# Optimization experiments

Measured on AMD Instinct MI355X. Metric: run time of the kernel, lower is better.

Reference implementation:

```python
import jax, jax.numpy as jnp
import numpy as np

THETA = 10000.0
NUM_HEADS = 16


def _rope(x, pos, theta):
    # x: [..., T, d_k], pos: [T]
    d_k = x.shape[-1]
    inv_freq = 1.0 / theta ** (jnp.arange(0, d_k, 2, dtype=jnp.float32) / d_k)
    ang = pos.astype(jnp.float32)[:, None] * inv_freq  # [T, d_k/2]
    cos, sin = jnp.cos(ang), jnp.sin(ang)
    x1, x2 = x[..., ::2], x[..., 1::2]
    even = x1 * cos - x2 * sin
    odd = x1 * sin + x2 * cos
    return jnp.stack([even, odd], axis=-1).reshape(x.shape)


def setup_inputs() -> dict:
    key = jax.random.key(0)
    ks = jax.random.split(key, 5)
    B, T, D = 4, 2048, 1024
    return {
        "in_features": jax.random.normal(ks[0], (B, T, D), dtype=jnp.float32),
        "token_positions": jnp.arange(T, dtype=jnp.int64 if jax.config.jax_enable_x64 else jnp.int32),
        "Wq": jax.random.normal(ks[1], (D, D), dtype=jnp.float32) * 0.02,
        "Wk": jax.random.normal(ks[2], (D, D), dtype=jnp.float32) * 0.02,
        "Wv": jax.random.normal(ks[3], (D, D), dtype=jnp.float32) * 0.02,
        "Wo": jax.random.normal(ks[4], (D, D), dtype=jnp.float32) * 0.02,
    }


def reference(in_features, token_positions, Wq, Wk, Wv, Wo):
    B, T, D = in_features.shape
    h = NUM_HEADS
    d_k = D // h
    # projections (weight stored [out, in], torch applies x @ W.T)
    Q = in_features @ Wq.T
    K = in_features @ Wk.T
    V = in_features @ Wv.T
    # [B, T, h*d_k] -> [B, h, T, d_k]
    Q = Q.reshape(B, T, h, d_k).transpose(0, 2, 1, 3)
    K = K.reshape(B, T, h, d_k).transpose(0, 2, 1, 3)
    V = V.reshape(B, T, h, d_k).transpose(0, 2, 1, 3)
    Q = _rope(Q, token_positions, THETA)
    K = _rope(K, token_positions, THETA)
    scores = jnp.einsum("bhqd,bhkd->bhqk", Q, K) / jnp.sqrt(jnp.float32(d_k))
    causal = jnp.tril(jnp.ones((T, T), dtype=bool))
    scores = jnp.where(causal, scores, -jnp.inf)
    attn = jax.nn.softmax(scores, axis=-1)
    heads = jnp.einsum("bhqk,bhkd->bhqd", attn, V)
    out = heads.transpose(0, 2, 1, 3).reshape(B, T, D)
    return out @ Wo.T
```

## Files before the change

kernel.cpp:

```cpp
#include <hip/hip_runtime.h>


typedef unsigned short u16;
typedef short short8 __attribute__((ext_vector_type(8)));
typedef float f32x4 __attribute__((ext_vector_type(4)));

#if defined(__has_builtin)
#if __has_builtin(__builtin_amdgcn_exp2f)
#define EXP2(x) __builtin_amdgcn_exp2f(x)
#else
#define EXP2(x) exp2f(x)
#endif
#else
#define EXP2(x) exp2f(x)
#endif

#define QSCALE 0.18033688011112042f
#define NEG_L2T_32 -0.4152410118609203f

__device__ __forceinline__ float bf2f(u16 u) {
  return __uint_as_float(((unsigned int)u) << 16);
}
__device__ __forceinline__ u16 f2bf(float f) {
  unsigned int x = __float_as_uint(f);
  x += 0x7fff + ((x >> 16) & 1);
  return (u16)(x >> 16);
}

__device__ __forceinline__ void glds16(const u16* g, u16* l) {
  __builtin_amdgcn_global_load_lds(
      (const __attribute__((address_space(1))) unsigned int*)g,
      (__attribute__((address_space(3))) unsigned int*)l, 16, 0, 0);
}

__global__ __launch_bounds__(256) void cvt_all(
    const float* __restrict__ X, const float* __restrict__ Wq,
    const float* __restrict__ Wk, const float* __restrict__ Wv,
    const float* __restrict__ Wo, u16* __restrict__ Xb,
    u16* __restrict__ Wqkvb, u16* __restrict__ Wob) {
  const int gid = blockIdx.x * 256 + threadIdx.x;
  const int i = gid * 8;
  const int M1 = 1 << 20;
  const float* src;
  u16* dst;
  int off;
  if (i < 8 * M1)        { src = X;  dst = Xb;            off = 0; }
  else if (i < 9 * M1)   { src = Wq; dst = Wqkvb;         off = 8 * M1; }
  else if (i < 10 * M1)  { src = Wk; dst = Wqkvb + M1;    off = 9 * M1; }
  else if (i < 11 * M1)  { src = Wv; dst = Wqkvb + 2*M1;  off = 10 * M1; }
  else                   { src = Wo; dst = Wob;           off = 11 * M1; }
  const int j = i - off;
  const float4 a = *(const float4*)(src + j);
  const float4 b = *(const float4*)(src + j + 4);
  short8 o;
  o[0] = (short)f2bf(a.x); o[1] = (short)f2bf(a.y);
  o[2] = (short)f2bf(a.z); o[3] = (short)f2bf(a.w);
  o[4] = (short)f2bf(b.x); o[5] = (short)f2bf(b.y);
  o[6] = (short)f2bf(b.z); o[7] = (short)f2bf(b.w);
  *(short8*)(dst + j) = o;
}

__global__ __launch_bounds__(256) void gemm_qkv(const u16* __restrict__ A,
                                                const u16* __restrict__ W,
                                                const int* __restrict__ pos,
                                                u16* __restrict__ Qr,
                                                u16* __restrict__ Kr,
                                                u16* __restrict__ Vd) {
  const int K = 1024;
  __shared__ __align__(16) u16 As[128 * 64];
  __shared__ __align__(16) u16 Bs[128 * 64];
  const int tid = threadIdx.x;
  const int m0 = blockIdx.y << 7;
  const int n0 = blockIdx.x << 7;
  const int w = tid >> 6, L = tid & 63;
  const int wm = (w >> 1) << 6, wn = (w & 1) << 6;
  const int lane15 = L & 15, quad = L >> 4;

  f32x4 acc[4][4] = {};

  const u16* Ap[4]; const u16* Bp[4];
  u16* Al[4]; u16* Bl[4];
#pragma unroll
  for (int i = 0; i < 4; ++i) {
    const int s = tid + (i << 8);
    const int row = s >> 3;
    const int c = ((s & 7) ^ (row & 7)) << 3;
    Ap[i] = A + (size_t)(m0 + row) * K + c;
    Bp[i] = W + (size_t)(n0 + row) * K + c;
    Al[i] = &As[s * 8];
    Bl[i] = &Bs[s * 8];
  }

  int offA[4][2], offB[4][2];
#pragma unroll
  for (int mt = 0; mt < 4; ++mt) {
    const int ra = wm + mt * 16 + lane15;
    const int rb = wn + mt * 16 + lane15;
    offA[mt][0] = ra * 64 + ((quad ^ (ra & 7)) << 3);
    offA[mt][1] = ra * 64 + (((quad + 4) ^ (ra & 7)) << 3);
    offB[mt][0] = rb * 64 + ((quad ^ (rb & 7)) << 3);
    offB[mt][1] = rb * 64 + (((quad + 4) ^ (rb & 7)) << 3);
  }

  for (int k0 = 0; k0 < K; k0 += 64) {
    __syncthreads();
#pragma unroll
    for (int i = 0; i < 4; ++i) glds16(Ap[i] + k0, Al[i]);
#pragma unroll
    for (int i = 0; i < 4; ++i) glds16(Bp[i] + k0, Bl[i]);
    __syncthreads();
#pragma unroll
    for (int ks = 0; ks < 2; ++ks) {
      short8 a[4], b[4];
#pragma unroll
      for (int mt = 0; mt < 4; ++mt) a[mt] = *(const short8*)&As[offA[mt][ks]];
#pragma unroll
      for (int nt = 0; nt < 4; ++nt) b[nt] = *(const short8*)&Bs[offB[nt][ks]];
#pragma unroll
      for (int mt = 0; mt < 4; ++mt)
#pragma unroll
        for (int nt = 0; nt < 4; ++nt)
          acc[mt][nt] =
              __builtin_amdgcn_mfma_f32_16x16x32_bf16(a[mt], b[nt], acc[mt][nt], 0, 0, 0);
    }
  }

  const int sel = n0 >> 10;
  const int ncol0 = (n0 & 1023) + wn;
  if (sel == 2) {
#pragma unroll
    for (int mt = 0; mt < 4; ++mt) {
      const int rbase = m0 + wm + mt * 16 + (quad << 2);
#pragma unroll
      for (int nt = 0; nt < 4; ++nt) {
        const int col = ncol0 + nt * 16 + lane15;
#pragma unroll
        for (int r = 0; r < 4; ++r)
          Vd[(size_t)(rbase + r) * 1024 + col] = f2bf(acc[mt][nt][r]);
      }
    }
  } else {
    u16* dst = sel ? Kr : Qr;
    const float sc = sel ? 1.0f : QSCALE;
    float invf[4];
#pragma unroll
    for (int nt = 0; nt < 4; ++nt) {
      const int d2 = ((ncol0 + nt * 16 + lane15) & 63) >> 1;
      invf[nt] = EXP2((float)d2 * NEG_L2T_32);
    }
#pragma unroll
    for (int mt = 0; mt < 4; ++mt) {
      const int rbase = m0 + wm + mt * 16 + (quad << 2);
#pragma unroll
      for (int r = 0; r < 4; ++r) {
        const int m = rbase + r;
        const int bb = m >> 11, tt = m & 2047;
        const float posf = (float)pos[tt];
#pragma unroll
        for (int nt = 0; nt < 4; ++nt) {
          const int col = ncol0 + nt * 16 + lane15;
          const int h = col >> 6, dcol = col & 63;
          float sn, cn;
          __sincosf(posf * invf[nt], &sn, &cn);
          const float self = acc[mt][nt][r];
          const float part = __shfl_xor(self, 1, 64);
          const float res = (dcol & 1) ? (part * sn + self * cn)
                                       : (self * cn - part * sn);
          dst[(((size_t)((bb * 16 + h) * 2048 + tt)) << 6) + dcol] = f2bf(res * sc);
        }
      }
    }
  }
}

__global__ __launch_bounds__(256) void gemm_bt(const u16* __restrict__ A,
                                               const u16* __restrict__ B,
                                               float* __restrict__ C,
                                               int M, int N, int K) {
  __shared__ __align__(16) u16 As[64 * 32];
  __shared__ __align__(16) u16 Bs[128 * 32];
  const int tid = threadIdx.x;
  const int m0 = blockIdx.y << 6;
  const int n0 = blockIdx.x << 7;
  const int w = tid >> 6, L = tid & 63;
  const int wm = (w >> 1) << 5, wn = (w & 1) << 6;
  const int lane15 = L & 15, quad = L >> 4;
  const int koff = quad << 3;

  f32x4 acc[2][4] = {};

  const int s0 = tid, s1 = tid + 256;
  const u16* A0 = A + (size_t)(m0 + (s0 >> 2)) * K + ((s0 & 3) << 3);
  const u16* B0 = B + (size_t)(n0 + (s0 >> 2)) * K + ((s0 & 3) << 3);
  const u16* B1 = B + (size_t)(n0 + (s1 >> 2)) * K + ((s1 & 3) << 3);
  u16* asd0 = &As[s0 * 8];
  u16* bsd0 = &Bs[s0 * 8]; u16* bsd1 = &Bs[s1 * 8];

  for (int k0 = 0; k0 < K; k0 += 32) {
    __syncthreads();
    glds16(A0 + k0, asd0);
    glds16(B0 + k0, bsd0);
    glds16(B1 + k0, bsd1);
    __syncthreads();
    short8 a[2], b[4];
#pragma unroll
    for (int mt = 0; mt < 2; ++mt)
      a[mt] = *(const short8*)&As[(wm + mt * 16 + lane15) * 32 + koff];
#pragma unroll
    for (int nt = 0; nt < 4; ++nt)
      b[nt] = *(const short8*)&Bs[(wn + nt * 16 + lane15) * 32 + koff];
#pragma unroll
    for (int mt = 0; mt < 2; ++mt)
#pragma unroll
      for (int nt = 0; nt < 4; ++nt)
        acc[mt][nt] =
            __builtin_amdgcn_mfma_f32_16x16x32_bf16(a[mt], b[nt], acc[mt][nt], 0, 0, 0);
  }

#pragma unroll
  for (int mt = 0; mt < 2; ++mt) {
    const int rbase = m0 + wm + mt * 16 + (quad << 2);
#pragma unroll
    for (int nt = 0; nt < 4; ++nt) {
      const int col = n0 + wn + nt * 16 + lane15;
#pragma unroll
      for (int r = 0; r < 4; ++r)
        C[(size_t)(rbase + r) * N + col] = acc[mt][nt][r];
    }
  }
}

__global__ __launch_bounds__(256) void transpose_v(const u16* __restrict__ Vlin,
                                                   u16* __restrict__ Vt) {
  __shared__ __align__(16) u16 tile[64][68];
  const int tid = threadIdx.x;
  const int bh = blockIdx.y, b = bh >> 4, h = bh & 15;
  const int t0 = blockIdx.x << 6;
#pragma unroll
  for (int i = 0; i < 4; ++i) {
    int s = tid + (i << 8);
    int tl = s >> 4, c4 = (s & 15) << 2;
    *(uint2*)&tile[tl][c4] =
        *(const uint2*)(Vlin + (((size_t)(b * 2048 + t0 + tl)) << 10) + (h << 6) + c4);
  }
  __syncthreads();
#pragma unroll
  for (int i = 0; i < 4; ++i) {
    int s = tid + (i << 8);
    int d = s >> 4, t4 = (s & 15) << 2;
    uint2 o;
    o.x = (unsigned)tile[t4 + 0][d] | ((unsigned)tile[t4 + 1][d] << 16);
    o.y = (unsigned)tile[t4 + 2][d] | ((unsigned)tile[t4 + 3][d] << 16);
    *(uint2*)(Vt + (((size_t)(bh * 64 + d)) << 11) + t0 + t4) = o;
  }
}

__global__ __launch_bounds__(256) void flash_attn(const u16* __restrict__ Q,
                                                  const u16* __restrict__ Kk,
                                                  const u16* __restrict__ Vt,
                                                  u16* __restrict__ O) {
  __shared__ __align__(16) u16 Ksm[64 * 72];
  __shared__ __align__(16) u16 Vsm[64 * 72];
  __shared__ __align__(16) u16 Psm[8][16 * 64];
  const int tid = threadIdx.x;
  const int w = tid >> 6, L = tid & 63;
  const int lane15 = L & 15, quad = L >> 4;
  const int qt = 15 - (blockIdx.x >> 6);
  const int bh = blockIdx.x & 63;
  const int b = bh >> 4, h = bh & 15;
  const int rq = lane15 >> 2;
  const int nkt = 2 * qt + 2;

  const int s0 = tid, s1 = tid + 256;
  const u16* kbase = Kk + ((size_t)bh << 17);
  const u16* kp0 = kbase + s0 * 8;
  const u16* kp1 = kbase + s1 * 8;
  const u16* vbase = Vt + ((size_t)bh << 17);
  const u16* vp0 = vbase + (size_t)(s0 >> 3) * 2048 + (s0 & 7) * 8;
  const u16* vp1 = vbase + (size_t)(s1 >> 3) * 2048 + (s1 & 7) * 8;
  const int d0 = (s0 >> 3) * 72 + (s0 & 7) * 8;
  const int d1 = (s1 >> 3) * 72 + (s1 & 7) * 8;

  const size_t qrow = (size_t)bh * 2048 + qt * 128 + w * 32;
  short8 qa[2][2];
#pragma unroll
  for (int hf = 0; hf < 2; ++hf) {
    const size_t qb = (qrow + hf * 16 + lane15) << 6;
    qa[hf][0] = *(const short8*)(Q + qb + (quad << 3));
    qa[hf][1] = *(const short8*)(Q + qb + 32 + (quad << 3));
  }

  uint4 kr0 = *(const uint4*)kp0;
  uint4 kr1 = *(const uint4*)kp1;
  uint4 vr0 = *(const uint4*)vp0;
  uint4 vr1 = *(const uint4*)vp1;
  *(uint4*)&Ksm[d0] = kr0; *(uint4*)&Ksm[d1] = kr1;
  *(uint4*)&Vsm[d0] = vr0; *(uint4*)&Vsm[d1] = vr1;
  __syncthreads();

  f32x4 o_acc[2][4] = {};
  float l_part[2][4] = {};

  for (int kt = 0; kt < nkt; ++kt) {
    if (kt + 1 < nkt) {
      kr0 = *(const uint4*)(kp0 + (size_t)(kt + 1) * 4096);
      kr1 = *(const uint4*)(kp1 + (size_t)(kt + 1) * 4096);
      vr0 = *(const uint4*)(vp0 + (kt + 1) * 64);
      vr1 = *(const uint4*)(vp1 + (kt + 1) * 64);
    }

    short8 kb[4][2];
#pragma unroll
    for (int nt = 0; nt < 4; ++nt) {
      kb[nt][0] = *(const short8*)&Ksm[(nt * 16 + lane15) * 72 + (quad << 3)];
      kb[nt][1] = *(const short8*)&Ksm[(nt * 16 + lane15) * 72 + 32 + (quad << 3)];
    }

#pragma unroll
    for (int hf = 0; hf < 2; ++hf) {
      const int B0 = qt * 128 + w * 32 + hf * 16;
      if (kt * 64 > B0 + 15) continue;
      u16* pw = Psm[w * 2 + hf];

      f32x4 sc[4];
#pragma unroll
      for (int nt = 0; nt < 4; ++nt) {
        f32x4 a = {};
        a = __builtin_amdgcn_mfma_f32_16x16x32_bf16(qa[hf][0], kb[nt][0], a, 0, 0, 0);
        a = __builtin_amdgcn_mfma_f32_16x16x32_bf16(qa[hf][1], kb[nt][1], a, 0, 0, 0);
        sc[nt] = a;
      }

      if (kt * 64 + 63 > B0) {
#pragma unroll
        for (int nt = 0; nt < 4; ++nt)
#pragma unroll
          for (int r = 0; r < 4; ++r) {
            const int row = B0 + (quad << 2) + r;
            const int key = kt * 64 + nt * 16 + lane15;
            if (key > row) sc[nt][r] = -1e30f;
          }
      }

      asm volatile("" ::: "memory");
#pragma unroll
      for (int nt = 0; nt < 4; ++nt) {
        const int colsw = ((nt ^ quad) << 4) + lane15;
#pragma unroll
        for (int r = 0; r < 4; ++r) {
          const float p = EXP2(sc[nt][r]);
          l_part[hf][r] += p;
          pw[((quad << 2) + r) * 64 + colsw] = (u16)(__float_as_uint(p) >> 16);
        }
      }
      asm volatile("" ::: "memory");

#pragma unroll
      for (int ks = 0; ks < 2; ++ks) {
        const short8 pa =
            *(const short8*)&pw[lane15 * 64 + ((ks * 32 + quad * 8) ^ (rq << 4))];
#pragma unroll
        for (int dt = 0; dt < 4; ++dt) {
          const short8 vb =
              *(const short8*)&Vsm[(dt * 16 + lane15) * 72 + ks * 32 + quad * 8];
          o_acc[hf][dt] =
              __builtin_amdgcn_mfma_f32_16x16x32_bf16(pa, vb, o_acc[hf][dt], 0, 0, 0);
        }
      }
    }

    if (kt + 1 < nkt) {
      __syncthreads();
      *(uint4*)&Ksm[d0] = kr0; *(uint4*)&Ksm[d1] = kr1;
      *(uint4*)&Vsm[d0] = vr0; *(uint4*)&Vsm[d1] = vr1;
      __syncthreads();
    }
  }

#pragma unroll
  for (int hf = 0; hf < 2; ++hf) {
#pragma unroll
    for (int r = 0; r < 4; ++r) {
      float l = l_part[hf][r];
#pragma unroll
      for (int off = 1; off < 16; off <<= 1) l += __shfl_xor(l, off, 64);
      const float inv = 1.f / l;
      const int t = qt * 128 + w * 32 + hf * 16 + (quad << 2) + r;
      const size_t obase = (((size_t)b * 2048 + t) << 10) + (h << 6);
#pragma unroll
      for (int dt = 0; dt < 4; ++dt)
        O[obase + dt * 16 + lane15] = f2bf(o_acc[hf][dt][r] * inv);
    }
  }
}

extern "C" void kernel_launch(void* const* d_in, const int* in_sizes, int n_in,
                              void* d_out, int out_size, void* d_ws, size_t ws_size,
                              hipStream_t stream) {
  const float* X  = (const float*)d_in[0];
  const int* pos  = (const int*)d_in[1];
  const float* Wq = (const float*)d_in[2];
  const float* Wk = (const float*)d_in[3];
  const float* Wv = (const float*)d_in[4];
  const float* Wo = (const float*)d_in[5];
  float* out = (float*)d_out;

  char* ws = (char*)d_ws;
  const size_t SZ = (size_t)8192 * 1024 * sizeof(u16);
  const size_t WSZ = (size_t)1024 * 1024 * sizeof(u16);
  u16* Vlin = (u16*)(ws + 0 * SZ);
  u16* Qr   = (u16*)(ws + 1 * SZ);
  u16* Kr   = (u16*)(ws + 2 * SZ);
  u16* Vt   = (u16*)(ws + 3 * SZ);
  u16* Xb   = (u16*)(ws + 4 * SZ);
  u16* Oh   = Vlin;
  char* wtail = ws + 5 * SZ;
  u16* Wqkvb = (u16*)(wtail);
  u16* Wob   = (u16*)(wtail + 3 * WSZ);

  const dim3 blk(256);

  cvt_all<<<6144, blk, 0, stream>>>(X, Wq, Wk, Wv, Wo, Xb, Wqkvb, Wob);
  gemm_qkv<<<dim3(24, 64), blk, 0, stream>>>(Xb, Wqkvb, pos, Qr, Kr, Vlin);
  transpose_v<<<dim3(32, 64), blk, 0, stream>>>(Vlin, Vt);
  flash_attn<<<1024, blk, 0, stream>>>(Qr, Kr, Vt, Oh);
  gemm_bt<<<dim3(8, 128), blk, 0, stream>>>(Oh, Wob, out, 8192, 1024, 1024);
}
```

Baseline: 271.1 us.

## Pair light and heavy causal query tiles per block and interleave PV MFMAs

Each attention block now handles two query tiles, g and 15-g, so every block does the same causal work, and the grid shrinks from 1024 to 512 blocks. Within each key tile, the P·V MFMAs for both 16-row halves are interleaved after both softmax passes instead of running one half after the other. This aims to remove tail imbalance across the grid and give more independent MFMAs per step. The cost is half as many blocks for occupancy and extra barriers between passes.

```diff
diff --git a/kernel.cpp b/kernel.cpp
--- a/kernel.cpp
+++ b/kernel.cpp
@@ -265,11 +265,10 @@
   const int tid = threadIdx.x;
   const int w = tid >> 6, L = tid & 63;
   const int lane15 = L & 15, quad = L >> 4;
-  const int qt = 15 - (blockIdx.x >> 6);
+  const int g = blockIdx.x >> 6;
   const int bh = blockIdx.x & 63;
   const int b = bh >> 4, h = bh & 15;
   const int rq = lane15 >> 2;
-  const int nkt = 2 * qt + 2;
 
   const int s0 = tid, s1 = tid + 256;
   const u16* kbase = Kk + ((size_t)bh << 17);
@@ -281,115 +280,139 @@
   const int d0 = (s0 >> 3) * 72 + (s0 & 7) * 8;
   const int d1 = (s1 >> 3) * 72 + (s1 & 7) * 8;
 
-  const size_t qrow = (size_t)bh * 2048 + qt * 128 + w * 32;
-  short8 qa[2][2];
-#pragma unroll
-  for (int hf = 0; hf < 2; ++hf) {
-    const size_t qb = (qrow + hf * 16 + lane15) << 6;
-    qa[hf][0] = *(const short8*)(Q + qb + (quad << 3));
-    qa[hf][1] = *(const short8*)(Q + qb + 32 + (quad << 3));
-  }
-
-  uint4 kr0 = *(const uint4*)kp0;
-  uint4 kr1 = *(const uint4*)kp1;
-  uint4 vr0 = *(const uint4*)vp0;
-  uint4 vr1 = *(const uint4*)vp1;
-  *(uint4*)&Ksm[d0] = kr0; *(uint4*)&Ksm[d1] = kr1;
-  *(uint4*)&Vsm[d0] = vr0; *(uint4*)&Vsm[d1] = vr1;
-  __syncthreads();
-
-  f32x4 o_acc[2][4] = {};
-  float l_part[2][4] = {};
-
-  for (int kt = 0; kt < nkt; ++kt) {
-    if (kt + 1 < nkt) {
-      kr0 = *(const uint4*)(kp0 + (size_t)(kt + 1) * 4096);
-      kr1 = *(const uint4*)(kp1 + (size_t)(kt + 1) * 4096);
-      vr0 = *(const uint4*)(vp0 + (kt + 1) * 64);
-      vr1 = *(const uint4*)(vp1 + (kt + 1) * 64);
-    }
-
-    short8 kb[4][2];
-#pragma unroll
-    for (int nt = 0; nt < 4; ++nt) {
-      kb[nt][0] = *(const short8*)&Ksm[(nt * 16 + lane15) * 72 + (quad << 3)];
-      kb[nt][1] = *(const short8*)&Ksm[(nt * 16 + lane15) * 72 + 32 + (quad << 3)];
-    }
-
+  for (int pass = 0; pass < 2; ++pass) {
+    const int qt = pass ? (15 - g) : g;
+    const int nkt = 2 * qt + 2;
+
+    const size_t qrow = (size_t)bh * 2048 + qt * 128 + w * 32;
+    short8 qa[2][2];
 #pragma unroll
     for (int hf = 0; hf < 2; ++hf) {
-      const int B0 = qt * 128 + w * 32 + hf * 16;
-      if (kt * 64 > B0 + 15) continue;
-      u16* pw = Psm[w * 2 + hf];
-
-      f32x4 sc[4];
+      const size_t qb = (qrow + hf * 16 + lane15) << 6;
+      qa[hf][0] = *(const short8*)(Q + qb + (quad << 3));
+      qa[hf][1] = *(const short8*)(Q + qb + 32 + (quad << 3));
+    }
+
+    uint4 kr0 = *(const uint4*)kp0;
+    uint4 kr1 = *(const uint4*)kp1;
+    uint4 vr0 = *(const uint4*)vp0;
+    uint4 vr1 = *(const uint4*)vp1;
+    __syncthreads();
+    *(uint4*)&Ksm[d0] = kr0; *(uint4*)&Ksm[d1] = kr1;
+    *(uint4*)&Vsm[d0] = vr0; *(uint4*)&Vsm[d1] = vr1;
+    __syncthreads();
+
+    f32x4 o_acc[2][4] = {};
+    float l_part[2][4] = {};
+    const int B0w = qt * 128 + w * 32;
+
+    for (int kt = 0; kt < nkt; ++kt) {
+      if (kt + 1 < nkt) {
+        kr0 = *(const uint4*)(kp0 + (size_t)(kt + 1) * 4096);
+        kr1 = *(const uint4*)(kp1 + (size_t)(kt + 1) * 4096);
+        vr0 = *(const uint4*)(vp0 + (kt + 1) * 64);
+        vr1 = *(const uint4*)(vp1 + (kt + 1) * 64);
+      }
+
+      short8 kb[4][2];
 #pragma unroll
       for (int nt = 0; nt < 4; ++nt) {
-        f32x4 a = {};
-        a = __builtin_amdgcn_mfma_f32_16x16x32_bf16(qa[hf][0], kb[nt][0], a, 0, 0, 0);
-        a = __builtin_amdgcn_mfma_f32_16x16x32_bf16(qa[hf][1], kb[nt][1], a, 0, 0, 0);
-        sc[nt] = a;
-      }
-
-      if (kt * 64 + 63 > B0) {
-#pragma unroll
-        for (int nt = 0; nt < 4; ++nt)
+        kb[nt][0] = *(const short8*)&Ksm[(nt * 16 + lane15) * 72 + (quad << 3)];
+        kb[nt][1] = *(const short8*)&Ksm[(nt * 16 + lane15) * 72 + 32 + (quad << 3)];
+      }
+
+      const bool act0 = (kt * 64 <= B0w + 15);
+      const bool act1 = (kt * 64 <= B0w + 31);
+
+#pragma unroll
+      for (int hf = 0; hf < 2; ++hf) {
+        const int B0 = B0w + hf * 16;
+        if (kt * 64 > B0 + 15) continue;
+        u16* pw = Psm[w * 2 + hf];
+
+        f32x4 sc[4];
+#pragma unroll
+        for (int nt = 0; nt < 4; ++nt) {
+          f32x4 a = {};
+          a = __builtin_amdgcn_mfma_f32_16x16x32_bf16(qa[hf][0], kb[nt][0], a, 0, 0, 0);
+          a = __builtin_amdgcn_mfma_f32_16x16x32_bf16(qa[hf][1], kb[nt][1], a, 0, 0, 0);
+          sc[nt] = a;
+        }
+
+        if (kt * 64 + 63 > B0) {
+#pragma unroll
+          for (int nt = 0; nt < 4; ++nt)
+#pragma unroll
+            for (int r = 0; r < 4; ++r) {
+              const int row = B0 + (quad << 2) + r;
+              const int key = kt * 64 + nt * 16 + lane15;
+              if (key > row) sc[nt][r] = -1e30f;
+            }
+        }
+
+#pragma unroll
+        for (int nt = 0; nt < 4; ++nt) {
+          const int colsw = ((nt ^ quad) << 4) + lane15;
 #pragma unroll
           for (int r = 0; r < 4; ++r) {
-            const int row = B0 + (quad << 2) + r;
-            const int key = kt * 64 + nt * 16 + lane15;
-            if (key > row) sc[nt][r] = -1e30f;
+            const float p = EXP2(sc[nt][r]);
+            l_part[hf][r] += p;
+            pw[((quad << 2) + r) * 64 + colsw] = (u16)(__float_as_uint(p) >> 16);
           }
-      }
-
+        }
+      }
       asm volatile("" ::: "memory");
-#pragma unroll
-      for (int nt = 0; nt < 4; ++nt) {
-        const int colsw = ((nt ^ quad) << 4) + lane15;
-#pragma unroll
-        for (int r = 0; r < 4; ++r) {
-          const float p = EXP2(sc[nt][r]);
-          l_part[hf][r] += p;
-          pw[((quad << 2) + r) * 64 + colsw] = (u16)(__float_as_uint(p) >> 16);
-        }
-      }
-      asm volatile("" ::: "memory");
-
+
+      short8 pa[2][2];
+      if (act0) {
+#pragma unroll
+        for (int ks = 0; ks < 2; ++ks)
+          pa[0][ks] = *(const short8*)&Psm[w * 2][lane15 * 64 +
+                                               ((ks * 32 + quad * 8) ^ (rq << 4))];
+      }
+      if (act1) {
+#pragma unroll
+        for (int ks = 0; ks < 2; ++ks)
+          pa[1][ks] = *(const short8*)&Psm[w * 2 + 1][lane15 * 64 +
+                                               ((ks * 32 + quad * 8) ^ (rq << 4))];
+      }
 #pragma unroll
       for (int ks = 0; ks < 2; ++ks) {
-        const short8 pa =
-            *(const short8*)&pw[lane15 * 64 + ((ks * 32 + quad * 8) ^ (rq << 4))];
 #pragma unroll
         for (int dt = 0; dt < 4; ++dt) {
           const short8 vb =
               *(const short8*)&Vsm[(dt * 16 + lane15) * 72 + ks * 32 + quad * 8];
-          o_acc[hf][dt] =
-              __builtin_amdgcn_mfma_f32_16x16x32_bf16(pa, vb, o_acc[hf][dt], 0, 0, 0);
+          if (act0)
+            o_acc[0][dt] =
+                __builtin_amdgcn_mfma_f32_16x16x32_bf16(pa[0][ks], vb, o_acc[0][dt], 0, 0, 0);
+          if (act1)
+            o_acc[1][dt] =
+                __builtin_amdgcn_mfma_f32_16x16x32_bf16(pa[1][ks], vb, o_acc[1][dt], 0, 0, 0);
         }
       }
-    }
-
-    if (kt + 1 < nkt) {
-      __syncthreads();
-      *(uint4*)&Ksm[d0] = kr0; *(uint4*)&Ksm[d1] = kr1;
-      *(uint4*)&Vsm[d0] = vr0; *(uint4*)&Vsm[d1] = vr1;
-      __syncthreads();
-    }
-  }
-
-#pragma unroll
-  for (int hf = 0; hf < 2; ++hf) {
-#pragma unroll
-    for (int r = 0; r < 4; ++r) {
-      float l = l_part[hf][r];
-#pragma unroll
-      for (int off = 1; off < 16; off <<= 1) l += __shfl_xor(l, off, 64);
-      const float inv = 1.f / l;
-      const int t = qt * 128 + w * 32 + hf * 16 + (quad << 2) + r;
-      const size_t obase = (((size_t)b * 2048 + t) << 10) + (h << 6);
-#pragma unroll
-      for (int dt = 0; dt < 4; ++dt)
-        O[obase + dt * 16 + lane15] = f2bf(o_acc[hf][dt][r] * inv);
+
+      if (kt + 1 < nkt) {
+        __syncthreads();
+        *(uint4*)&Ksm[d0] = kr0; *(uint4*)&Ksm[d1] = kr1;
+        *(uint4*)&Vsm[d0] = vr0; *(uint4*)&Vsm[d1] = vr1;
+        __syncthreads();
+      }
+    }
+
+#pragma unroll
+    for (int hf = 0; hf < 2; ++hf) {
+#pragma unroll
+      for (int r = 0; r < 4; ++r) {
+        float l = l_part[hf][r];
+#pragma unroll
+        for (int off = 1; off < 16; off <<= 1) l += __shfl_xor(l, off, 64);
+        const float inv = 1.f / l;
+        const int t = qt * 128 + w * 32 + hf * 16 + (quad << 2) + r;
+        const size_t obase = (((size_t)b * 2048 + t) << 10) + (h << 6);
+#pragma unroll
+        for (int dt = 0; dt < 4; ++dt)
+          O[obase + dt * 16 + lane15] = f2bf(o_acc[hf][dt][r] * inv);
+      }
     }
   }
 }
@@ -423,6 +446,6 @@
   cvt_all<<<6144, blk, 0, stream>>>(X, Wq, Wk, Wv, Wo, Xb, Wqkvb, Wob);
   gemm_qkv<<<dim3(24, 64), blk, 0, stream>>>(Xb, Wqkvb, pos, Qr, Kr, Vlin);
   transpose_v<<<dim3(32, 64), blk, 0, stream>>>(Vlin, Vt);
-  flash_attn<<<1024, blk, 0, stream>>>(Qr, Kr, Vt, Oh);
+  flash_attn<<<512, blk, 0, stream>>>(Qr, Kr, Vt, Oh);
   gemm_bt<<<dim3(8, 128), blk, 0, stream>>>(Oh, Wob, out, 8192, 1024, 1024);
 }
```

Result: no change. 271.4 us (+0.1%).
